# Optimization experiments

Measured on AMD Instinct MI355X. Metric: run time of the kernel, lower is better.

Reference implementation:

```python
import jax, jax.numpy as jnp
import numpy as np

N_NODES = 100000
N_EDGES = 1600000
D_IN = 64
D_OUT = 64


def setup_inputs() -> dict:
    key = jax.random.key(0)
    k1, k2, k3, k4, k5 = jax.random.split(key, 5)
    feat = jax.random.normal(k1, (N_NODES, D_IN), dtype=jnp.float32)
    src = jax.random.randint(k2, (N_EDGES,), 0, N_NODES, dtype=jnp.int64)
    dst = jax.random.randint(k3, (N_EDGES,), 0, N_NODES, dtype=jnp.int64)
    s = 1.0 / np.sqrt(D_IN)
    W_self = jax.random.uniform(k4, (D_IN, D_OUT), dtype=jnp.float32, minval=-s, maxval=s)
    W_neigh = jax.random.uniform(k5, (D_IN, D_OUT), dtype=jnp.float32, minval=-s, maxval=s)
    bias = jnp.zeros((D_OUT,), dtype=jnp.float32)
    return {"feat": feat, "src": src, "dst": dst, "W_self": W_self, "W_neigh": W_neigh, "bias": bias}


def reference(feat, src, dst, W_self, W_neigh, bias):
    # SAGEConv with mean aggregation: gather source feats, scatter-add to dst,
    # divide by in-degree (clamped to 1 for isolated nodes, as DGL does).
    n = feat.shape[0]
    neigh_sum = jax.ops.segment_sum(feat[src], dst, num_segments=n)  # [N, D_IN]
    deg = jax.ops.segment_sum(jnp.ones_like(dst, dtype=feat.dtype), dst, num_segments=n)
    h_neigh = neigh_sum / jnp.maximum(deg, 1.0)[:, None]
    out = feat @ W_self + h_neigh @ W_neigh + bias  # [N, D_OUT]
    return jax.nn.relu(out)
```

## Files before the change

kernel.cpp:

```cpp
#include <hip/hip_runtime.h>

#define N_NODES 100000
#define N_EDGES 1600000
#define D 64
#define SLOTS 64

#define NBUCK 512
#define BSZ   196
#define CAP   3584
#define NBLK  512
#define EPB   (N_EDGES / NBLK)

__device__ __forceinline__ unsigned short f2bf(float x) {
    unsigned u = __float_as_uint(x);
    unsigned r = u + 0x7FFFu + ((u >> 16) & 1u);
    return (unsigned short)(r >> 16);
}
__device__ __forceinline__ float bf2f(unsigned short u) {
    return __uint_as_float(((unsigned)u) << 16);
}

__global__ __launch_bounds__(256) void cast_kernel(
    const float* __restrict__ feat, unsigned short* __restrict__ featb)
{
    int i = blockIdx.x * 256 + threadIdx.x;
    if (i < N_NODES * D / 4) {
        float4 v = reinterpret_cast<const float4*>(feat)[i];
        ushort4 o;
        o.x = f2bf(v.x); o.y = f2bf(v.y); o.z = f2bf(v.z); o.w = f2bf(v.w);
        reinterpret_cast<ushort4*>(featb)[i] = o;
    }
}

__global__ __launch_bounds__(NBUCK) void init_kernel(int* __restrict__ gcur)
{
    gcur[threadIdx.x] = threadIdx.x * CAP;
}

__global__ __launch_bounds__(256) void scatter_kernel(
    const int* __restrict__ src, const int* __restrict__ dst,
    int* __restrict__ gcur, unsigned* __restrict__ sorted)
{
    __shared__ int lh[NBUCK];
    __shared__ int bb[NBUCK];
    __shared__ int lcur[NBUCK];
    int t = threadIdx.x;
    #pragma unroll
    for (int i = t; i < NBUCK; i += 256) lh[i] = 0;
    __syncthreads();
    int base = blockIdx.x * EPB;
    for (int i = base + t; i < base + EPB; i += 256)
        atomicAdd(&lh[dst[i] / BSZ], 1);
    __syncthreads();
    #pragma unroll
    for (int i = t; i < NBUCK; i += 256) {
        bb[i] = lh[i] ? atomicAdd(&gcur[i], lh[i]) : 0;
        lcur[i] = 0;
    }
    __syncthreads();
    for (int i = base + t; i < base + EPB; i += 256) {
        int d = dst[i];
        int b = d / BSZ;
        int p = atomicAdd(&lcur[b], 1);
        int pos = bb[b] + p;
        if (pos < (b + 1) * CAP)
            sorted[pos] = ((unsigned)src[i] << 9) | (unsigned)(d - b * BSZ);
    }
}

__global__ __launch_bounds__(1024) void bucket_agg_kernel(
    const unsigned short* __restrict__ featb,
    const unsigned* __restrict__ sorted,
    const int* __restrict__ gcur,
    float* __restrict__ h)
{
    __shared__ int lcnt[BSZ];
    __shared__ int lslots[BSZ * SLOTS];

    int t = threadIdx.x;
    for (int i = t; i < BSZ; i += 1024) lcnt[i] = 0;
    __syncthreads();

    int b  = blockIdx.x;
    int es = b * CAP;
    int cnt = gcur[b] - es;
    if (cnt > CAP) cnt = CAP;
    int ee = es + cnt;

    for (int i = es + t; i < ee; i += 1024) {
        unsigned pk = sorted[i];
        int dl = (int)(pk & 511u);
        int p = atomicAdd(&lcnt[dl], 1);
        if (p < SLOTS) lslots[dl * SLOTS + p] = (int)(pk >> 9);
    }
    __syncthreads();

    int w    = t >> 6;
    int lane = t & 63;
    int eg   = lane >> 4;
    int c    = lane & 15;
    int gbase = b * BSZ;

    for (int ln = w; ln < BSZ; ln += 16) {
        int gn = gbase + ln;
        if (gn >= N_NODES) break;
        int deg = lcnt[ln];
        int lim = deg < SLOTS ? deg : SLOTS;
        float4 acc = make_float4(0.f, 0.f, 0.f, 0.f);
        for (int k = eg; k < lim; k += 4) {
            int s = lslots[ln * SLOTS + k];
            const ushort4 u = *reinterpret_cast<const ushort4*>(
                featb + (size_t)s * D + (c << 2));
            acc.x += bf2f(u.x); acc.y += bf2f(u.y);
            acc.z += bf2f(u.z); acc.w += bf2f(u.w);
        }
        acc.x += __shfl_xor(acc.x, 16, 64);
        acc.y += __shfl_xor(acc.y, 16, 64);
        acc.z += __shfl_xor(acc.z, 16, 64);
        acc.w += __shfl_xor(acc.w, 16, 64);
        acc.x += __shfl_xor(acc.x, 32, 64);
        acc.y += __shfl_xor(acc.y, 32, 64);
        acc.z += __shfl_xor(acc.z, 32, 64);
        acc.w += __shfl_xor(acc.w, 32, 64);
        if (eg == 0) {
            float inv = 1.0f / fmaxf((float)deg, 1.0f);
            float4 r = make_float4(acc.x * inv, acc.y * inv,
                                   acc.z * inv, acc.w * inv);
            *reinterpret_cast<float4*>(h + (size_t)gn * D + (c << 2)) = r;
        }
    }
}

#define EP_CHUNK 16
#define PD (D + 4)

__global__ __launch_bounds__(256) void epilogue_kernel(
    const float* __restrict__ feat,
    const float* __restrict__ Wself,
    const float* __restrict__ Wneigh,
    const float* __restrict__ bias,
    float* __restrict__ out)
{
    __shared__ float sWs[D * D];
    __shared__ float sWn[D * D];
    __shared__ float sF[EP_CHUNK][PD];
    __shared__ float sH[EP_CHUNK][PD];

    int t = threadIdx.x;
    #pragma unroll
    for (int i = 0; i < (D * D) / 256; ++i) {
        int idx = t + i * 256;
        sWs[idx] = Wself[idx];
        sWn[idx] = Wneigh[idx];
    }
    int li = t >> 4;
    int jj = t & 15;
    const float4 b4 = *reinterpret_cast<const float4*>(bias + jj * 4);
    __syncthreads();

    const int nchunks = (N_NODES + EP_CHUNK - 1) / EP_CHUNK;
    for (int ch = blockIdx.x; ch < nchunks; ch += gridDim.x) {
        int node = ch * EP_CHUNK + li;
        if (node < N_NODES) {
            *reinterpret_cast<float4*>(&sF[li][jj * 4]) =
                *reinterpret_cast<const float4*>(feat + (size_t)node * D + jj * 4);
            *reinterpret_cast<float4*>(&sH[li][jj * 4]) =
                *reinterpret_cast<const float4*>(out + (size_t)node * D + jj * 4);
        }
        __syncthreads();
        if (node < N_NODES) {
            float4 acc = b4;
            #pragma unroll
            for (int i = 0; i < D; ++i) {
                float f  = sF[li][i];
                float hh = sH[li][i];
                const float4 ws = *reinterpret_cast<const float4*>(&sWs[i * D + jj * 4]);
                const float4 wn = *reinterpret_cast<const float4*>(&sWn[i * D + jj * 4]);
                acc.x = fmaf(f, ws.x, fmaf(hh, wn.x, acc.x));
                acc.y = fmaf(f, ws.y, fmaf(hh, wn.y, acc.y));
                acc.z = fmaf(f, ws.z, fmaf(hh, wn.z, acc.z));
                acc.w = fmaf(f, ws.w, fmaf(hh, wn.w, acc.w));
            }
            acc.x = fmaxf(acc.x, 0.f);
            acc.y = fmaxf(acc.y, 0.f);
            acc.z = fmaxf(acc.z, 0.f);
            acc.w = fmaxf(acc.w, 0.f);
            *reinterpret_cast<float4*>(out + (size_t)node * D + jj * 4) = acc;
        }
        __syncthreads();
    }
}

extern "C" void kernel_launch(void* const* d_in, const int* in_sizes, int n_in,
                              void* d_out, int out_size, void* d_ws, size_t ws_size,
                              hipStream_t stream)
{
    const float* feat   = (const float*)d_in[0];
    const int*   src    = (const int*)d_in[1];
    const int*   dst    = (const int*)d_in[2];
    const float* Wself  = (const float*)d_in[3];
    const float* Wneigh = (const float*)d_in[4];
    const float* bias   = (const float*)d_in[5];
    float* out = (float*)d_out;

    int*            gcur   = (int*)d_ws;
    unsigned*       sorted = (unsigned*)((int*)d_ws + 1024);
    unsigned short* featb  = (unsigned short*)(sorted + (size_t)NBUCK * CAP);

    cast_kernel<<<(N_NODES * D / 4 + 255) / 256, 256, 0, stream>>>(feat, featb);
    init_kernel<<<1, NBUCK, 0, stream>>>(gcur);
    scatter_kernel<<<NBLK, 256, 0, stream>>>(src, dst, gcur, sorted);

    bucket_agg_kernel<<<NBUCK, 1024, 0, stream>>>(featb, sorted, gcur, out);

    epilogue_kernel<<<1024, 256, 0, stream>>>(feat, Wself, Wneigh, bias, out);
}
```

Before: 196.6 us.

## Replace FP32 epilogue GEMM with bf16 MFMA using prepacked weights

```diff
diff --git a/kernel.cpp b/kernel.cpp
--- a/kernel.cpp
+++ b/kernel.cpp
@@ -10,6 +10,9 @@
 #define CAP   3584
 #define NBLK  512
 #define EPB   (N_EDGES / NBLK)
+
+typedef __attribute__((ext_vector_type(8))) short bf16x8;
+typedef __attribute__((ext_vector_type(4))) float f32x4;
 
 __device__ __forceinline__ unsigned short f2bf(float x) {
     unsigned u = __float_as_uint(x);
@@ -30,6 +33,25 @@
         o.x = f2bf(v.x); o.y = f2bf(v.y); o.z = f2bf(v.z); o.w = f2bf(v.w);
         reinterpret_cast<ushort4*>(featb)[i] = o;
     }
+}
+
+__global__ __launch_bounds__(1024) void wpack_kernel(
+    const float* __restrict__ Ws, const float* __restrict__ Wn,
+    unsigned short* __restrict__ wp)
+{
+    int t = threadIdx.x;
+    int m  = t >> 9;
+    int kt = (t >> 8) & 1;
+    int jt = (t >> 6) & 3;
+    int l  = t & 63;
+    const float* W = m ? Wn : Ws;
+    int kbase = kt * 32 + (l >> 4) * 8;
+    int col   = jt * 16 + (l & 15);
+    unsigned short v[8];
+    #pragma unroll
+    for (int e = 0; e < 8; ++e)
+        v[e] = f2bf(W[(kbase + e) * D + col]);
+    *reinterpret_cast<uint4*>(wp + (size_t)t * 8) = *reinterpret_cast<const uint4*>(v);
 }
 
 __global__ __launch_bounds__(NBUCK) void init_kernel(int* __restrict__ gcur)
@@ -131,63 +153,68 @@
     }
 }
 
-#define EP_CHUNK 16
-#define PD (D + 4)
-
-__global__ __launch_bounds__(256) void epilogue_kernel(
-    const float* __restrict__ feat,
-    const float* __restrict__ Wself,
-    const float* __restrict__ Wneigh,
+__global__ __launch_bounds__(256) void epilogue_mfma_kernel(
+    const unsigned short* __restrict__ featb,
+    const unsigned short* __restrict__ wp,
     const float* __restrict__ bias,
     float* __restrict__ out)
 {
-    __shared__ float sWs[D * D];
-    __shared__ float sWn[D * D];
-    __shared__ float sF[EP_CHUNK][PD];
-    __shared__ float sH[EP_CHUNK][PD];
-
-    int t = threadIdx.x;
-    #pragma unroll
-    for (int i = 0; i < (D * D) / 256; ++i) {
-        int idx = t + i * 256;
-        sWs[idx] = Wself[idx];
-        sWn[idx] = Wneigh[idx];
-    }
-    int li = t >> 4;
-    int jj = t & 15;
-    const float4 b4 = *reinterpret_cast<const float4*>(bias + jj * 4);
-    __syncthreads();
-
-    const int nchunks = (N_NODES + EP_CHUNK - 1) / EP_CHUNK;
-    for (int ch = blockIdx.x; ch < nchunks; ch += gridDim.x) {
-        int node = ch * EP_CHUNK + li;
-        if (node < N_NODES) {
-            *reinterpret_cast<float4*>(&sF[li][jj * 4]) =
-                *reinterpret_cast<const float4*>(feat + (size_t)node * D + jj * 4);
-            *reinterpret_cast<float4*>(&sH[li][jj * 4]) =
-                *reinterpret_cast<const float4*>(out + (size_t)node * D + jj * 4);
-        }
-        __syncthreads();
-        if (node < N_NODES) {
-            float4 acc = b4;
+    int l    = threadIdx.x & 63;
+    int krow = l >> 4;
+    int col  = l & 15;
+    int wid  = (blockIdx.x << 2) + (threadIdx.x >> 6);
+    const int NW = gridDim.x << 2;
+
+    bf16x8 bws[2][4], bwn[2][4];
+    #pragma unroll
+    for (int kt = 0; kt < 2; ++kt)
+        #pragma unroll
+        for (int jt = 0; jt < 4; ++jt) {
+            bws[kt][jt] = *reinterpret_cast<const bf16x8*>(
+                wp + (size_t)(((0 * 2 + kt) * 4 + jt) * 64 + l) * 8);
+            bwn[kt][jt] = *reinterpret_cast<const bf16x8*>(
+                wp + (size_t)(((1 * 2 + kt) * 4 + jt) * 64 + l) * 8);
+        }
+    float bv[4];
+    #pragma unroll
+    for (int jt = 0; jt < 4; ++jt) bv[jt] = bias[jt * 16 + col];
+
+    const int NCHUNK = N_NODES / 16;
+    for (int ch = wid; ch < NCHUNK; ch += NW) {
+        int arow = ch * 16 + col;
+        bf16x8 af[2], ah[2];
+        #pragma unroll
+        for (int kt = 0; kt < 2; ++kt) {
+            const size_t ko = (size_t)arow * D + kt * 32 + krow * 8;
+            af[kt] = *reinterpret_cast<const bf16x8*>(featb + ko);
+            const float4 h0 = *reinterpret_cast<const float4*>(out + ko);
+            const float4 h1 = *reinterpret_cast<const float4*>(out + ko + 4);
+            bf16x8 a;
+            a[0] = (short)f2bf(h0.x); a[1] = (short)f2bf(h0.y);
+            a[2] = (short)f2bf(h0.z); a[3] = (short)f2bf(h0.w);
+            a[4] = (short)f2bf(h1.x); a[5] = (short)f2bf(h1.y);
+            a[6] = (short)f2bf(h1.z); a[7] = (short)f2bf(h1.w);
+            ah[kt] = a;
+        }
+        f32x4 acc[4];
+        #pragma unroll
+        for (int jt = 0; jt < 4; ++jt) acc[jt] = (f32x4){0.f, 0.f, 0.f, 0.f};
+        #pragma unroll
+        for (int jt = 0; jt < 4; ++jt)
             #pragma unroll
-            for (int i = 0; i < D; ++i) {
-                float f  = sF[li][i];
-                float hh = sH[li][i];
-                const float4 ws = *reinterpret_cast<const float4*>(&sWs[i * D + jj * 4]);
-                const float4 wn = *reinterpret_cast<const float4*>(&sWn[i * D + jj * 4]);
-                acc.x = fmaf(f, ws.x, fmaf(hh, wn.x, acc.x));
-                acc.y = fmaf(f, ws.y, fmaf(hh, wn.y, acc.y));
-                acc.z = fmaf(f, ws.z, fmaf(hh, wn.z, acc.z));
-                acc.w = fmaf(f, ws.w, fmaf(hh, wn.w, acc.w));
+            for (int kt = 0; kt < 2; ++kt) {
+                acc[jt] = __builtin_amdgcn_mfma_f32_16x16x32_bf16(
+                    af[kt], bws[kt][jt], acc[jt], 0, 0, 0);
+                acc[jt] = __builtin_amdgcn_mfma_f32_16x16x32_bf16(
+                    ah[kt], bwn[kt][jt], acc[jt], 0, 0, 0);
             }
-            acc.x = fmaxf(acc.x, 0.f);
-            acc.y = fmaxf(acc.y, 0.f);
-            acc.z = fmaxf(acc.z, 0.f);
-            acc.w = fmaxf(acc.w, 0.f);
-            *reinterpret_cast<float4*>(out + (size_t)node * D + jj * 4) = acc;
-        }
-        __syncthreads();
+        int orow0 = ch * 16 + krow * 4;
+        #pragma unroll
+        for (int jt = 0; jt < 4; ++jt)
+            #pragma unroll
+            for (int r = 0; r < 4; ++r)
+                out[(size_t)(orow0 + r) * D + jt * 16 + col] =
+                    fmaxf(acc[jt][r] + bv[jt], 0.f);
     }
 }
 
@@ -206,12 +233,14 @@
     int*            gcur   = (int*)d_ws;
     unsigned*       sorted = (unsigned*)((int*)d_ws + 1024);
     unsigned short* featb  = (unsigned short*)(sorted + (size_t)NBUCK * CAP);
+    unsigned short* wpk    = featb + (size_t)N_NODES * D;
 
     cast_kernel<<<(N_NODES * D / 4 + 255) / 256, 256, 0, stream>>>(feat, featb);
+    wpack_kernel<<<1, 1024, 0, stream>>>(Wself, Wneigh, wpk);
     init_kernel<<<1, NBUCK, 0, stream>>>(gcur);
     scatter_kernel<<<NBLK, 256, 0, stream>>>(src, dst, gcur, sorted);
 
     bucket_agg_kernel<<<NBUCK, 1024, 0, stream>>>(featb, sorted, gcur, out);
 
-    epilogue_kernel<<<1024, 256, 0, stream>>>(feat, Wself, Wneigh, bias, out);
-}
+    epilogue_mfma_kernel<<<1024, 256, 0, stream>>>(featb, wpk, bias, out);
+}
```

After: 173.8 us. 11.6% less time.
